# Kernel tuning notes

Hardware: AMD Instinct MI355X
Metric: run time of the kernel (lower is better)

## Reference

```python
import jax, jax.numpy as jnp
import numpy as np

# Sizes (see shape_source): B=4, N1=8192, N2=4096, T=H1=15, E1=131072, E2=65536
# conv1: Fin=1, G1=64, K=12, H=15 (collapse_H=True -> temporal dim folds to 1)
# conv2: Fin=64, G2=32, K=12, H=1

def _cheb_norm(src, dst, w, n):
    # Scaled Laplacian with lambda_max=2 (PyG ChebConv sym norm): L_hat = -D^{-1/2} A D^{-1/2}
    deg = jax.ops.segment_sum(w, dst, num_segments=n)
    dinv = jnp.where(deg > 0, 1.0 / jnp.sqrt(deg), 0.0)
    return -w * dinv[src] * dinv[dst]

def _prop(h, src, dst, norm, n):
    # h: (N, D, B) -> (L_hat h): (N, D, B) via edge gather + segment-sum scatter
    return jax.ops.segment_sum(norm[:, None, None] * h[src], dst, num_segments=n)

def _cheb_time_conv(h, src, dst, norm, W, b, n):
    # Chebyshev recursion: T0=x, T1=L_hat x, Tk = 2 L_hat T_{k-1} - T_{k-2}
    # h: (N, D, B); W: (K, D, G); output (N, G, B). D folds temporal H and Fin.
    K = W.shape[0]
    y = jnp.einsum('ndb,dg->ngb', h, W[0])
    Tx_prev = h
    Tx_cur = _prop(h, src, dst, norm, n)
    y = y + jnp.einsum('ndb,dg->ngb', Tx_cur, W[1])
    for k in range(2, K):
        Tx_next = 2.0 * _prop(Tx_cur, src, dst, norm, n) - Tx_prev
        y = y + jnp.einsum('ndb,dg->ngb', Tx_next, W[k])
        Tx_prev, Tx_cur = Tx_cur, Tx_next
    return y + b[None, :, None]

def setup_inputs() -> dict:
    key = jax.random.key(0)
    ks = jax.random.split(key, 12)
    B, N1, N2, T = 4, 8192, 4096, 15
    E1, E2 = 131072, 65536
    K, G1, G2, C = 12, 64, 32, 6
    return {
        'x': jax.random.normal(ks[0], (B, N1, T), dtype=jnp.float32),
        'edge_index1': jax.random.randint(ks[1], (2, E1), 0, N1, dtype=jnp.int64),
        'edge_weight1': jax.random.uniform(ks[2], (E1,), dtype=jnp.float32),
        'edge_index2': jax.random.randint(ks[3], (2, E2), 0, N2, dtype=jnp.int64),
        'edge_weight2': jax.random.uniform(ks[4], (E2,), dtype=jnp.float32),
        'b_map': jax.random.normal(ks[5], (N2, N1), dtype=jnp.float32) * 0.02,
        'W1': jax.random.normal(ks[6], (K, T, 1, G1), dtype=jnp.float32) * 0.1,
        'b1': jax.random.normal(ks[7], (G1,), dtype=jnp.float32) * 0.1,
        'W2': jax.random.normal(ks[8], (K, 1, G1, G2), dtype=jnp.float32) * 0.05,
        'b2': jax.random.normal(ks[9], (G2,), dtype=jnp.float32) * 0.1,
        'fc_w': jax.random.normal(ks[10], (C, N2 * G2), dtype=jnp.float32) * 0.01,
        'fc_b': jax.random.normal(ks[11], (C,), dtype=jnp.float32) * 0.1,
    }

def reference(x, edge_index1, edge_weight1, edge_index2, edge_weight2,
              b_map, W1, b1, W2, b2, fc_w, fc_b):
    Bsz = x.shape[0]
    h = jnp.transpose(x, (1, 2, 0))                      # torch x.permute(1,2,0): (N1, T, B)
    n1 = h.shape[0]
    s1, d1 = edge_index1[0], edge_index1[1]
    norm1 = _cheb_norm(s1, d1, edge_weight1, n1)
    # conv1: collapse_H folds the whole T=H window -> (N1, G1, B)
    h = _cheb_time_conv(h, s1, d1, norm1, W1.reshape(W1.shape[0], -1, W1.shape[-1]), b1, n1)
    h = jax.nn.relu(h)
    # temporal/pooling mapping: torch.matmul(b, x.permute(2,3,0,1)).permute(2,3,0,1)
    h = jnp.einsum('mn,ngb->mgb', b_map, h)              # (N2, G1, B)
    n2 = h.shape[0]
    s2, d2 = edge_index2[0], edge_index2[1]
    norm2 = _cheb_norm(s2, d2, edge_weight2, n2)
    h = _cheb_time_conv(h, s2, d2, norm2, W2.reshape(W2.shape[0], -1, W2.shape[-1]), b2, n2)  # (N2, G2, B)
    # faithful torch .view(B, -1) on contiguous (N2, G2, 1, B)
    flat = jnp.reshape(h[:, :, None, :], (Bsz, -1))
    logits = flat @ fc_w.T + fc_b
    return jax.nn.log_softmax(logits, axis=1)
```

## Files before the change

### kernel.cpp

```cpp
#include <hip/hip_runtime.h>

#define NB   4
#define NN1  8192
#define TT   15
#define NN2  4096
#define KCH  12
#define GG1  64
#define GG2  32
#define NCLS 6
#define EE1  131072
#define EE2  65536

typedef __attribute__((ext_vector_type(8))) short bf16x8;
typedef __attribute__((ext_vector_type(4))) float f32x4;

__device__ inline short f2bf(float f) {
    unsigned u = __builtin_bit_cast(unsigned, f);
    u += 0x7FFFu + ((u >> 16) & 1u);
    return (short)(u >> 16);
}

__global__ void k_deg_hist(const int* __restrict__ ei, const float* __restrict__ w,
                           float* __restrict__ deg, int* __restrict__ cnt, int E) {
    int e = blockIdx.x * 256 + threadIdx.x;
    if (e < E) {
        int d = ei[E + e];
        atomicAdd(&deg[d], w[e]);
        atomicAdd(&cnt[d], 1);
    }
}

template <int N>
__global__ __launch_bounds__(1024) void k_scan(const int* __restrict__ cnt,
                                               int* __restrict__ offs, int* __restrict__ cur) {
    constexpr int PER = N / 1024;
    __shared__ int part[1024];
    int t = threadIdx.x;
    int loc[PER];
    int s = 0;
#pragma unroll
    for (int i = 0; i < PER; ++i) { loc[i] = s; s += cnt[t * PER + i]; }
    part[t] = s;
    __syncthreads();
    for (int off = 1; off < 1024; off <<= 1) {
        int v = (t >= off) ? part[t - off] : 0;
        __syncthreads();
        part[t] += v;
        __syncthreads();
    }
    int pre = t ? part[t - 1] : 0;
#pragma unroll
    for (int i = 0; i < PER; ++i) { int v = pre + loc[i]; offs[t * PER + i] = v; cur[t * PER + i] = v; }
    if (t == 1023) offs[N] = part[1023];
}

__global__ void k_fill(const int* __restrict__ ei, const float* __restrict__ w,
                       const float* __restrict__ deg, int* __restrict__ cur,
                       int* __restrict__ csrc, float* __restrict__ cnrm, int E) {
    int e = blockIdx.x * 256 + threadIdx.x;
    if (e < E) {
        int s = ei[e], d = ei[E + e];
        float ds = deg[s], dd = deg[d];
        float is = ds > 0.f ? 1.f / sqrtf(ds) : 0.f;
        float id = dd > 0.f ? 1.f / sqrtf(dd) : 0.f;
        int p = atomicAdd(&cur[d], 1);
        csrc[p] = s;
        cnrm[p] = -w[e] * is * id;
    }
}

__global__ void k_build_h0(const float* __restrict__ x, float* __restrict__ h0,
                           short* __restrict__ bf0) {
    int idx = blockIdx.x * 256 + threadIdx.x;
    if (idx < NN1 * 64) {
        int n = idx >> 6, r = idx & 63;
        float v = 0.f;
        if (r < 60) {
            int t = r >> 2, b = r & 3;
            v = x[(b * NN1 + n) * TT + t];
        }
        h0[idx] = v;
        bf0[(size_t)n * 768 + r] = f2bf(v);
    }
}

__global__ __launch_bounds__(64) void k_prop1(const float* __restrict__ hprev,
                                              const float* __restrict__ hprev2,
                                              float* __restrict__ hout, short* __restrict__ bfs,
                                              const int* __restrict__ offs,
                                              const int* __restrict__ csrc,
                                              const float* __restrict__ cnrm, int first) {
    int n = blockIdx.x;
    int lane = threadIdx.x;
    int es = lane >> 4, f4 = lane & 15;
    int e0 = offs[n], e1 = offs[n + 1];
    f32x4 acc = {0.f, 0.f, 0.f, 0.f};
    for (int e = e0 + es; e < e1; e += 4) {
        int s = csrc[e];
        float wv = cnrm[e];
        const float4 v = *(const float4*)(hprev + (size_t)s * 64 + f4 * 4);
        acc[0] = fmaf(wv, v.x, acc[0]);
        acc[1] = fmaf(wv, v.y, acc[1]);
        acc[2] = fmaf(wv, v.z, acc[2]);
        acc[3] = fmaf(wv, v.w, acc[3]);
    }
#pragma unroll
    for (int i = 0; i < 4; ++i) {
        acc[i] += __shfl_xor(acc[i], 16, 64);
        acc[i] += __shfl_xor(acc[i], 32, 64);
    }
    if (es == 0) {
        float4 t;
        if (first) {
            t = make_float4(acc[0], acc[1], acc[2], acc[3]);
        } else {
            float4 p = *(const float4*)(hprev2 + (size_t)n * 64 + f4 * 4);
            t = make_float4(2.f * acc[0] - p.x, 2.f * acc[1] - p.y,
                            2.f * acc[2] - p.z, 2.f * acc[3] - p.w);
        }
        *(float4*)(hout + (size_t)n * 64 + f4 * 4) = t;
        short4 s4;
        s4.x = f2bf(t.x); s4.y = f2bf(t.y); s4.z = f2bf(t.z); s4.w = f2bf(t.w);
        *(short4*)(bfs + (size_t)n * 768 + f4 * 4) = s4;
    }
}

__global__ __launch_bounds__(256) void k_prop2(const float* __restrict__ hprev,
                                               const float* __restrict__ hprev2,
                                               float* __restrict__ hout, short* __restrict__ bfs,
                                               const int* __restrict__ offs,
                                               const int* __restrict__ csrc,
                                               const float* __restrict__ cnrm, int first) {
    __shared__ f32x4 red[3][64];
    int n = blockIdx.x;
    int t = threadIdx.x;
    int w = t >> 6, lane = t & 63;
    int e0 = offs[n], e1 = offs[n + 1];
    f32x4 acc = {0.f, 0.f, 0.f, 0.f};
    for (int e = e0 + w; e < e1; e += 4) {
        int s = csrc[e];
        float wv = cnrm[e];
        const float4 v = *(const float4*)(hprev + (size_t)s * 256 + lane * 4);
        acc[0] = fmaf(wv, v.x, acc[0]);
        acc[1] = fmaf(wv, v.y, acc[1]);
        acc[2] = fmaf(wv, v.z, acc[2]);
        acc[3] = fmaf(wv, v.w, acc[3]);
    }
    if (w) red[w - 1][lane] = acc;
    __syncthreads();
    if (w == 0) {
        f32x4 s = acc + red[0][lane] + red[1][lane] + red[2][lane];
        float4 tt;
        if (first) {
            tt = make_float4(s[0], s[1], s[2], s[3]);
        } else {
            float4 p = *(const float4*)(hprev2 + (size_t)n * 256 + lane * 4);
            tt = make_float4(2.f * s[0] - p.x, 2.f * s[1] - p.y,
                             2.f * s[2] - p.z, 2.f * s[3] - p.w);
        }
        *(float4*)(hout + (size_t)n * 256 + lane * 4) = tt;
        short4 s4;
        s4.x = f2bf(tt.x); s4.y = f2bf(tt.y); s4.z = f2bf(tt.z); s4.w = f2bf(tt.w);
        *(short4*)(bfs + (size_t)n * 3072 + lane * 4) = s4;
    }
}

__global__ void k_w1p(const float* __restrict__ W1, short* __restrict__ W1p) {
    int idx = blockIdx.x * 256 + threadIdx.x;
    if (idx < 256 * 768) {
        int j = idx / 768, d = idx - j * 768;
        int g = j >> 2, b = j & 3;
        int k = d >> 6, r = d & 63, t = r >> 2, bp = r & 3;
        float v = (b == bp && t < TT) ? W1[k * (TT * GG1) + t * GG1 + g] : 0.f;
        W1p[idx] = f2bf(v);
    }
}
__global__ void k_w2p(const float* __restrict__ W2, short* __restrict__ W2p) {
    int idx = blockIdx.x * 256 + threadIdx.x;
    if (idx < 128 * 3072) {
        int j = idx / 3072, d = idx - j * 3072;
        int g = j >> 2, b = j & 3;
        int k = d >> 8, r = d & 255, G = r >> 2, bp = r & 3;
        float v = (b == bp) ? W2[k * (GG1 * GG2) + G * GG2 + g] : 0.f;
        W2p[idx] = f2bf(v);
    }
}

template <bool A_BF, bool Y1EPI>
__global__ __launch_bounds__(256) void k_gemm(const void* __restrict__ Ap, int lda,
                                              const short* __restrict__ Bp, int ldb,
                                              const float* __restrict__ bias,
                                              float* __restrict__ Cf, int ldc,
                                              short* __restrict__ yT,
                                              int Kc, size_t pstride) {
    __shared__ short As[2][64][64];
    __shared__ short Bs[2][64][64];
    int m0 = blockIdx.x * 64, j0 = blockIdx.y * 64;
    int z = blockIdx.z;
    int kbeg = z * Kc;
    float* C = Cf + (size_t)z * pstride;
    int t = threadIdx.x;
    int lane = t & 63, wid = t >> 6;
    int wm = (wid >> 1) * 32, wn = (wid & 1) * 32;
    int lc = lane & 15, kg = lane >> 4;
    int r4 = t >> 2, c4 = (t & 3) * 16;
    int swa = (r4 & 7) << 3;

    const float* apf = (const float*)Ap + (size_t)(m0 + r4) * lda + kbeg + (t & 3) * 4;
    const short* apb = (const short*)Ap + (size_t)(m0 + r4) * lda + kbeg + c4;
    const short* bp  = Bp + (size_t)(j0 + r4) * ldb + kbeg + c4;

    float4 af0, af1, af2, af3;
    bf16x8 ab0, ab1, bb0, bb1;

    auto load_tile = [&](int k0) {
        if (A_BF) {
            ab0 = *(const bf16x8*)(apb + k0);
            ab1 = *(const bf16x8*)(apb + k0 + 8);
        } else {
            af0 = *(const float4*)(apf + k0);
            af1 = *(const float4*)(apf + k0 + 16);
            af2 = *(const float4*)(apf + k0 + 32);
            af3 = *(const float4*)(apf + k0 + 48);
        }
        bb0 = *(const bf16x8*)(bp + k0);
        bb1 = *(const bf16x8*)(bp + k0 + 8);
    };
    auto write_tile = [&](int buf) {
        if (A_BF) {
            *(bf16x8*)&As[buf][r4][c4 ^ swa] = ab0;
            *(bf16x8*)&As[buf][r4][(c4 + 8) ^ swa] = ab1;
        } else {
            short4 s;
            s.x = f2bf(af0.x); s.y = f2bf(af0.y); s.z = f2bf(af0.z); s.w = f2bf(af0.w);
            *(short4*)&As[buf][r4][((t & 3) * 4) ^ swa] = s;
            s.x = f2bf(af1.x); s.y = f2bf(af1.y); s.z = f2bf(af1.z); s.w = f2bf(af1.w);
            *(short4*)&As[buf][r4][((t & 3) * 4 + 16) ^ swa] = s;
            s.x = f2bf(af2.x); s.y = f2bf(af2.y); s.z = f2bf(af2.z); s.w = f2bf(af2.w);
            *(short4*)&As[buf][r4][((t & 3) * 4 + 32) ^ swa] = s;
            s.x = f2bf(af3.x); s.y = f2bf(af3.y); s.z = f2bf(af3.z); s.w = f2bf(af3.w);
            *(short4*)&As[buf][r4][((t & 3) * 4 + 48) ^ swa] = s;
        }
        *(bf16x8*)&Bs[buf][r4][c4 ^ swa] = bb0;
        *(bf16x8*)&Bs[buf][r4][(c4 + 8) ^ swa] = bb1;
    };

    f32x4 acc[2][2] = {};
    const int NIT = Kc >> 6;
    load_tile(0);
    write_tile(0);
    __syncthreads();
    for (int it = 0; it < NIT; ++it) {
        int cur = it & 1;
        if (it + 1 < NIT) load_tile((it + 1) << 6);
#pragma unroll
        for (int ks = 0; ks < 2; ++ks) {
            int kk = ks * 32 + kg * 8;
            bf16x8 a[2], b[2];
#pragma unroll
            for (int mi = 0; mi < 2; ++mi) {
                int row = wm + mi * 16 + lc;
                a[mi] = *(bf16x8*)&As[cur][row][kk ^ ((row & 7) << 3)];
            }
#pragma unroll
            for (int ni = 0; ni < 2; ++ni) {
                int row = wn + ni * 16 + lc;
                b[ni] = *(bf16x8*)&Bs[cur][row][kk ^ ((row & 7) << 3)];
            }
#pragma unroll
            for (int mi = 0; mi < 2; ++mi)
#pragma unroll
                for (int ni = 0; ni < 2; ++ni)
                    acc[mi][ni] = __builtin_amdgcn_mfma_f32_16x16x32_bf16(a[mi], b[ni], acc[mi][ni], 0, 0, 0);
        }
        if (it + 1 < NIT) write_tile(cur ^ 1);
        __syncthreads();
    }

    if (Y1EPI) {
#pragma unroll
        for (int mi = 0; mi < 2; ++mi)
#pragma unroll
            for (int ni = 0; ni < 2; ++ni) {
                int col = j0 + wn + ni * 16 + lc;
                float bb = bias[col >> 2];
                int row = m0 + wm + mi * 16 + kg * 4;
                short4 s;
                s.x = f2bf(fmaxf(acc[mi][ni][0] + bb, 0.f));
                s.y = f2bf(fmaxf(acc[mi][ni][1] + bb, 0.f));
                s.z = f2bf(fmaxf(acc[mi][ni][2] + bb, 0.f));
                s.w = f2bf(fmaxf(acc[mi][ni][3] + bb, 0.f));
                *(short4*)(yT + (size_t)col * NN1 + row) = s;
            }
    } else {
#pragma unroll
        for (int mi = 0; mi < 2; ++mi)
#pragma unroll
            for (int ni = 0; ni < 2; ++ni)
#pragma unroll
                for (int r = 0; r < 4; ++r) {
                    int row = m0 + wm + mi * 16 + kg * 4 + r, col = j0 + wn + ni * 16 + lc;
                    C[(size_t)row * ldc + col] = acc[mi][ni][r];
                }
    }
}

__global__ void k_red8(const float* __restrict__ part, float* __restrict__ Cf,
                       short* __restrict__ Cbf) {
    int i = blockIdx.x * 256 + threadIdx.x;
    if (i < NN2 * 64) {
        const float4* p = (const float4*)part + i;
        float4 s = p[0];
#pragma unroll
        for (int z = 1; z < 8; ++z) {
            float4 v = p[(size_t)z * NN2 * 64];
            s.x += v.x; s.y += v.y; s.z += v.z; s.w += v.w;
        }
        ((float4*)Cf)[i] = s;
        int n = i >> 6, col = (i & 63) * 4;
        short4 s4;
        s4.x = f2bf(s.x); s4.y = f2bf(s.y); s4.z = f2bf(s.z); s4.w = f2bf(s.w);
        *(short4*)(Cbf + (size_t)n * 3072 + col) = s4;
    }
}
__global__ void k_red4(const float* __restrict__ part, float* __restrict__ Cf) {
    int i = blockIdx.x * 256 + threadIdx.x;
    if (i < NN2 * 32) {
        const float4* p = (const float4*)part + i;
        float4 s = p[0];
#pragma unroll
        for (int z = 1; z < 4; ++z) {
            float4 v = p[(size_t)z * NN2 * 32];
            s.x += v.x; s.y += v.y; s.z += v.z; s.w += v.w;
        }
        ((float4*)Cf)[i] = s;
    }
}

__global__ __launch_bounds__(256) void k_fc(const float* __restrict__ y2, const float* __restrict__ b2,
                                            const float* __restrict__ fcw, float* __restrict__ logits) {
    int qc = blockIdx.x >> 4, ch = blockIdx.x & 15;
    int q = qc / NCLS, c = qc % NCLS;
    const float* yp = y2 + (size_t)q * 131072 + ch * 8192;
    const float* wp = fcw + (size_t)c * 131072 + ch * 8192;
    int t = threadIdx.x;
    float acc = 0.f;
#pragma unroll
    for (int it = 0; it < 8; ++it) {
        int o = it * 1024 + t * 4;
        float4 yv = *(const float4*)(yp + o);
        float4 wv = *(const float4*)(wp + o);
        float bg = b2[((ch * 8192 + o) >> 2) & 31];
        acc += (yv.x + bg) * wv.x + (yv.y + bg) * wv.y + (yv.z + bg) * wv.z + (yv.w + bg) * wv.w;
    }
#pragma unroll
    for (int o = 32; o; o >>= 1) acc += __shfl_down(acc, o, 64);
    __shared__ float red[4];
    if ((t & 63) == 0) red[t >> 6] = acc;
    __syncthreads();
    if (t == 0) atomicAdd(&logits[qc], red[0] + red[1] + red[2] + red[3]);
}

__global__ void k_lsm(const float* __restrict__ logits, const float* __restrict__ fcb,
                      float* __restrict__ out) {
    int q = threadIdx.x;
    if (q < NB) {
        float v[NCLS];
#pragma unroll
        for (int c = 0; c < NCLS; ++c) v[c] = logits[q * NCLS + c] + fcb[c];
        float m = -1e30f;
#pragma unroll
        for (int c = 0; c < NCLS; ++c) m = fmaxf(m, v[c]);
        float s = 0.f;
#pragma unroll
        for (int c = 0; c < NCLS; ++c) s += expf(v[c] - m);
        float lse = m + logf(s);
#pragma unroll
        for (int c = 0; c < NCLS; ++c) out[q * NCLS + c] = v[c] - lse;
    }
}

extern "C" void kernel_launch(void* const* d_in, const int* in_sizes, int n_in,
                              void* d_out, int out_size, void* d_ws, size_t ws_size,
                              hipStream_t stream) {
    const float* x    = (const float*)d_in[0];
    const int*   ei1  = (const int*)d_in[1];
    const float* ew1  = (const float*)d_in[2];
    const int*   ei2  = (const int*)d_in[3];
    const float* ew2  = (const float*)d_in[4];
    const float* bmap = (const float*)d_in[5];
    const float* W1   = (const float*)d_in[6];
    const float* b1   = (const float*)d_in[7];
    const float* W2   = (const float*)d_in[8];
    const float* b2   = (const float*)d_in[9];
    const float* fcw  = (const float*)d_in[10];
    const float* fcb  = (const float*)d_in[11];
    float* out = (float*)d_out;

    char* w = (char*)d_ws;
    size_t o = 0;
    auto alloc = [&](size_t bytes) {
        char* p = w + o;
        o += (bytes + 255) & ~(size_t)255;
        return p;
    };
    float* deg1  = (float*)alloc(NN1 * 4);
    float* deg2  = (float*)alloc(NN2 * 4);
    int*   cnt1  = (int*)alloc(NN1 * 4);
    int*   cnt2  = (int*)alloc(NN2 * 4);
    int*   offs1 = (int*)alloc((NN1 + 1) * 4);
    int*   offs2 = (int*)alloc((NN2 + 1) * 4);
    int*   cur1  = (int*)alloc(NN1 * 4);
    int*   cur2  = (int*)alloc(NN2 * 4);
    int*   csrc1 = (int*)alloc(EE1 * 4);
    float* cnrm1 = (float*)alloc(EE1 * 4);
    int*   csrc2 = (int*)alloc(EE2 * 4);
    float* cnrm2 = (float*)alloc(EE2 * 4);
    float* R1a = (float*)alloc(NN1 * 64 * 4);
    float* R1b = (float*)alloc(NN1 * 64 * 4);
    float* R1c = (float*)alloc(NN1 * 64 * 4);
    short* T1bf = (short*)alloc((size_t)NN1 * 768 * 2);
    short* ybfT = (short*)alloc((size_t)256 * NN1 * 2);
    float* R2a = (float*)alloc((size_t)NN2 * 256 * 4);
    float* R2b = (float*)alloc((size_t)NN2 * 256 * 4);
    float* R2c = (float*)alloc((size_t)NN2 * 256 * 4);
    short* T2bf = (short*)alloc((size_t)NN2 * 3072 * 2);
    float* y2  = (float*)alloc((size_t)NN2 * 128 * 4);
    short* W1p = (short*)alloc(256 * 768 * 2);
    short* W2p = (short*)alloc(128 * 3072 * 2);
    float* part8 = (float*)alloc((size_t)8 * NN2 * 256 * 4);
    float* part4 = (float*)alloc((size_t)4 * NN2 * 128 * 4);
    float* logits = (float*)alloc(256);

    hipMemsetAsync(deg1, 0, NN1 * 4, stream);
    hipMemsetAsync(deg2, 0, NN2 * 4, stream);
    hipMemsetAsync(cnt1, 0, NN1 * 4, stream);
    hipMemsetAsync(cnt2, 0, NN2 * 4, stream);
    hipMemsetAsync(logits, 0, 256, stream);
    k_deg_hist<<<EE1 / 256, 256, 0, stream>>>(ei1, ew1, deg1, cnt1, EE1);
    k_deg_hist<<<EE2 / 256, 256, 0, stream>>>(ei2, ew2, deg2, cnt2, EE2);
    k_scan<NN1><<<1, 1024, 0, stream>>>(cnt1, offs1, cur1);
    k_scan<NN2><<<1, 1024, 0, stream>>>(cnt2, offs2, cur2);
    k_fill<<<EE1 / 256, 256, 0, stream>>>(ei1, ew1, deg1, cur1, csrc1, cnrm1, EE1);
    k_fill<<<EE2 / 256, 256, 0, stream>>>(ei2, ew2, deg2, cur2, csrc2, cnrm2, EE2);

    k_w1p<<<(256 * 768) / 256, 256, 0, stream>>>(W1, W1p);
    k_w2p<<<(128 * 3072) / 256, 256, 0, stream>>>(W2, W2p);

    k_build_h0<<<(NN1 * 64) / 256, 256, 0, stream>>>(x, R1a, T1bf);
    {
        float *Tm1 = R1a, *Tm2 = nullptr, *fr = R1b, *spare = R1c;
        for (int k = 1; k < KCH; ++k) {
            k_prop1<<<NN1, 64, 0, stream>>>(Tm1, k == 1 ? Tm1 : Tm2, fr,
                                            T1bf + k * 64, offs1, csrc1, cnrm1, k == 1 ? 1 : 0);
            float* nf = (k == 1) ? spare : Tm2;
            Tm2 = Tm1; Tm1 = fr; fr = nf;
        }
    }
    {
        dim3 g(NN1 / 64, 256 / 64, 1);
        k_gemm<true, true><<<g, 256, 0, stream>>>(T1bf, 768, W1p, 768, b1,
                                                  nullptr, 0, ybfT, 768, 0);
    }
    {
        dim3 g(NN2 / 64, 256 / 64, 8);
        k_gemm<false, false><<<g, 256, 0, stream>>>(bmap, NN1, ybfT, NN1, nullptr,
                                                    part8, 256, nullptr, 1024, (size_t)NN2 * 256);
        k_red8<<<(NN2 * 64 + 255) / 256, 256, 0, stream>>>(part8, R2a, T2bf);
    }
    {
        float *Tm1 = R2a, *Tm2 = nullptr, *fr = R2b, *spare = R2c;
        for (int k = 1; k < KCH; ++k) {
            k_prop2<<<NN2, 256, 0, stream>>>(Tm1, k == 1 ? Tm1 : Tm2, fr,
                                             T2bf + k * 256, offs2, csrc2, cnrm2, k == 1 ? 1 : 0);
            float* nf = (k == 1) ? spare : Tm2;
            Tm2 = Tm1; Tm1 = fr; fr = nf;
        }
    }
    {
        dim3 g(NN2 / 64, 128 / 64, 4);
        k_gemm<true, false><<<g, 256, 0, stream>>>(T2bf, 3072, W2p, 3072, nullptr,
                                                   part4, 128, nullptr, 768, (size_t)NN2 * 128);
        k_red4<<<(NN2 * 32 + 255) / 256, 256, 0, stream>>>(part4, y2);
    }

    k_fc<<<NB * NCLS * 16, 256, 0, stream>>>(y2, b2, fcw, logits);
    k_lsm<<<1, 64, 0, stream>>>(logits, fcb, out);
}
```

Before: 555.3 us.

## Add 128x128 double-buffered MFMA GEMM for b_map mapping, pack node propagation kernels

Replaces the generic 64x64 GEMM for the dense b_map x conv1 output product with a dedicated 128x128 tile kernel. It converts fp32 A to bf16 on the fly, double-buffers LDS with an XOR swizzle, and prefetches the next K tile into registers during the MFMA work, which raises data reuse and hides load latency. The propagation kernels now pack four nodes per 256-thread block. k_prop2 handles one node per wave with a 2-way unrolled edge loop instead of splitting edges across waves and reducing through LDS. The tradeoff is higher register pressure in the big-tile GEMM and less edge-level parallelism per node in prop2.

New measurement: 559.3 us. No clear change (+0.7%).

```diff
diff --git a/kernel.cpp b/kernel.cpp
--- a/kernel.cpp
+++ b/kernel.cpp
@@ -18,6 +18,12 @@
     unsigned u = __builtin_bit_cast(unsigned, f);
     u += 0x7FFFu + ((u >> 16) & 1u);
     return (short)(u >> 16);
+}
+__device__ inline bf16x8 cvt8(float4 a, float4 b) {
+    bf16x8 r;
+    r[0] = f2bf(a.x); r[1] = f2bf(a.y); r[2] = f2bf(a.z); r[3] = f2bf(a.w);
+    r[4] = f2bf(b.x); r[5] = f2bf(b.y); r[6] = f2bf(b.z); r[7] = f2bf(b.w);
+    return r;
 }
 
 __global__ void k_deg_hist(const int* __restrict__ ei, const float* __restrict__ w,
@@ -84,14 +90,14 @@
     }
 }
 
-__global__ __launch_bounds__(64) void k_prop1(const float* __restrict__ hprev,
-                                              const float* __restrict__ hprev2,
-                                              float* __restrict__ hout, short* __restrict__ bfs,
-                                              const int* __restrict__ offs,
-                                              const int* __restrict__ csrc,
-                                              const float* __restrict__ cnrm, int first) {
-    int n = blockIdx.x;
-    int lane = threadIdx.x;
+__global__ __launch_bounds__(256) void k_prop1(const float* __restrict__ hprev,
+                                               const float* __restrict__ hprev2,
+                                               float* __restrict__ hout, short* __restrict__ bfs,
+                                               const int* __restrict__ offs,
+                                               const int* __restrict__ csrc,
+                                               const float* __restrict__ cnrm, int first) {
+    int n = blockIdx.x * 4 + (threadIdx.x >> 6);
+    int lane = threadIdx.x & 63;
     int es = lane >> 4, f4 = lane & 15;
     int e0 = offs[n], e1 = offs[n + 1];
     f32x4 acc = {0.f, 0.f, 0.f, 0.f};
@@ -131,38 +137,41 @@
                                                const int* __restrict__ offs,
                                                const int* __restrict__ csrc,
                                                const float* __restrict__ cnrm, int first) {
-    __shared__ f32x4 red[3][64];
-    int n = blockIdx.x;
-    int t = threadIdx.x;
-    int w = t >> 6, lane = t & 63;
+    int n = blockIdx.x * 4 + (threadIdx.x >> 6);
+    int lane = threadIdx.x & 63;
     int e0 = offs[n], e1 = offs[n + 1];
-    f32x4 acc = {0.f, 0.f, 0.f, 0.f};
-    for (int e = e0 + w; e < e1; e += 4) {
-        int s = csrc[e];
-        float wv = cnrm[e];
-        const float4 v = *(const float4*)(hprev + (size_t)s * 256 + lane * 4);
-        acc[0] = fmaf(wv, v.x, acc[0]);
-        acc[1] = fmaf(wv, v.y, acc[1]);
-        acc[2] = fmaf(wv, v.z, acc[2]);
-        acc[3] = fmaf(wv, v.w, acc[3]);
-    }
-    if (w) red[w - 1][lane] = acc;
-    __syncthreads();
-    if (w == 0) {
-        f32x4 s = acc + red[0][lane] + red[1][lane] + red[2][lane];
-        float4 tt;
-        if (first) {
-            tt = make_float4(s[0], s[1], s[2], s[3]);
-        } else {
-            float4 p = *(const float4*)(hprev2 + (size_t)n * 256 + lane * 4);
-            tt = make_float4(2.f * s[0] - p.x, 2.f * s[1] - p.y,
-                             2.f * s[2] - p.z, 2.f * s[3] - p.w);
-        }
-        *(float4*)(hout + (size_t)n * 256 + lane * 4) = tt;
-        short4 s4;
-        s4.x = f2bf(tt.x); s4.y = f2bf(tt.y); s4.z = f2bf(tt.z); s4.w = f2bf(tt.w);
-        *(short4*)(bfs + (size_t)n * 3072 + lane * 4) = s4;
-    }
+    f32x4 a0 = {0.f, 0.f, 0.f, 0.f}, a1 = {0.f, 0.f, 0.f, 0.f};
+    int e = e0;
+    for (; e + 1 < e1; e += 2) {
+        int s0 = csrc[e], s1 = csrc[e + 1];
+        float w0 = cnrm[e], w1 = cnrm[e + 1];
+        float4 v0 = *(const float4*)(hprev + (size_t)s0 * 256 + lane * 4);
+        float4 v1 = *(const float4*)(hprev + (size_t)s1 * 256 + lane * 4);
+        a0[0] = fmaf(w0, v0.x, a0[0]); a0[1] = fmaf(w0, v0.y, a0[1]);
+        a0[2] = fmaf(w0, v0.z, a0[2]); a0[3] = fmaf(w0, v0.w, a0[3]);
+        a1[0] = fmaf(w1, v1.x, a1[0]); a1[1] = fmaf(w1, v1.y, a1[1]);
+        a1[2] = fmaf(w1, v1.z, a1[2]); a1[3] = fmaf(w1, v1.w, a1[3]);
+    }
+    if (e < e1) {
+        int s0 = csrc[e];
+        float w0 = cnrm[e];
+        float4 v0 = *(const float4*)(hprev + (size_t)s0 * 256 + lane * 4);
+        a0[0] = fmaf(w0, v0.x, a0[0]); a0[1] = fmaf(w0, v0.y, a0[1]);
+        a0[2] = fmaf(w0, v0.z, a0[2]); a0[3] = fmaf(w0, v0.w, a0[3]);
+    }
+    f32x4 s = a0 + a1;
+    float4 tt;
+    if (first) {
+        tt = make_float4(s[0], s[1], s[2], s[3]);
+    } else {
+        float4 p = *(const float4*)(hprev2 + (size_t)n * 256 + lane * 4);
+        tt = make_float4(2.f * s[0] - p.x, 2.f * s[1] - p.y,
+                         2.f * s[2] - p.z, 2.f * s[3] - p.w);
+    }
+    *(float4*)(hout + (size_t)n * 256 + lane * 4) = tt;
+    short4 s4;
+    s4.x = f2bf(tt.x); s4.y = f2bf(tt.y); s4.z = f2bf(tt.z); s4.w = f2bf(tt.w);
+    *(short4*)(bfs + (size_t)n * 3072 + lane * 4) = s4;
 }
 
 __global__ void k_w1p(const float* __restrict__ W1, short* __restrict__ W1p) {
@@ -303,6 +312,87 @@
                     C[(size_t)row * ldc + col] = acc[mi][ni][r];
                 }
     }
+}
+
+__global__ __launch_bounds__(256) void k_gemm128(const float* __restrict__ Ap,
+                                                 const short* __restrict__ Bp,
+                                                 float* __restrict__ Cf,
+                                                 int Kc, size_t pstride) {
+    __shared__ short As[2][128][64];
+    __shared__ short Bs[2][128][64];
+    int m0 = blockIdx.x * 128, j0 = blockIdx.y * 128;
+    int z = blockIdx.z;
+    int kbeg = z * Kc;
+    float* C = Cf + (size_t)z * pstride;
+    int t = threadIdx.x;
+    int lane = t & 63, wid = t >> 6;
+    int wr = (wid >> 1) * 64, wc = (wid & 1) * 64;
+    int lc = lane & 15, kg = lane >> 4;
+    int rs = t >> 1;
+    int hb = (t & 1) * 32;
+    int swa = (rs & 7) << 3;
+
+    const float* ap = Ap + (size_t)(m0 + rs) * NN1 + kbeg + hb;
+    const short* bp = Bp + (size_t)(j0 + rs) * NN1 + kbeg + hb;
+
+    float4 af[8];
+    bf16x8 bb[4];
+    auto load_tile = [&](int k0) {
+#pragma unroll
+        for (int q = 0; q < 8; ++q) af[q] = *(const float4*)(ap + k0 + q * 4);
+#pragma unroll
+        for (int q = 0; q < 4; ++q) bb[q] = *(const bf16x8*)(bp + k0 + q * 8);
+    };
+    auto write_tile = [&](int buf) {
+#pragma unroll
+        for (int q = 0; q < 4; ++q)
+            *(bf16x8*)&As[buf][rs][(hb + q * 8) ^ swa] = cvt8(af[2 * q], af[2 * q + 1]);
+#pragma unroll
+        for (int q = 0; q < 4; ++q)
+            *(bf16x8*)&Bs[buf][rs][(hb + q * 8) ^ swa] = bb[q];
+    };
+
+    f32x4 acc[4][4] = {};
+    const int NIT = Kc >> 6;
+    load_tile(0);
+    write_tile(0);
+    __syncthreads();
+    for (int it = 0; it < NIT; ++it) {
+        int cur = it & 1;
+        if (it + 1 < NIT) load_tile((it + 1) << 6);
+#pragma unroll
+        for (int ks = 0; ks < 2; ++ks) {
+            int kk = ks * 32 + kg * 8;
+            bf16x8 a[4], b[4];
+#pragma unroll
+            for (int mi = 0; mi < 4; ++mi) {
+                int row = wr + mi * 16 + lc;
+                a[mi] = *(bf16x8*)&As[cur][row][kk ^ ((row & 7) << 3)];
+            }
+#pragma unroll
+            for (int ni = 0; ni < 4; ++ni) {
+                int row = wc + ni * 16 + lc;
+                b[ni] = *(bf16x8*)&Bs[cur][row][kk ^ ((row & 7) << 3)];
+            }
+#pragma unroll
+            for (int mi = 0; mi < 4; ++mi)
+#pragma unroll
+                for (int ni = 0; ni < 4; ++ni)
+                    acc[mi][ni] = __builtin_amdgcn_mfma_f32_16x16x32_bf16(a[mi], b[ni], acc[mi][ni], 0, 0, 0);
+        }
+        if (it + 1 < NIT) write_tile(cur ^ 1);
+        __syncthreads();
+    }
+#pragma unroll
+    for (int mi = 0; mi < 4; ++mi)
+#pragma unroll
+        for (int ni = 0; ni < 4; ++ni)
+#pragma unroll
+            for (int r = 0; r < 4; ++r) {
+                int row = m0 + wr + mi * 16 + kg * 4 + r;
+                int col = j0 + wc + ni * 16 + lc;
+                C[(size_t)row * 256 + col] = acc[mi][ni][r];
+            }
 }
 
 __global__ void k_red8(const float* __restrict__ part, float* __restrict__ Cf,
@@ -451,8 +541,8 @@
     {
         float *Tm1 = R1a, *Tm2 = nullptr, *fr = R1b, *spare = R1c;
         for (int k = 1; k < KCH; ++k) {
-            k_prop1<<<NN1, 64, 0, stream>>>(Tm1, k == 1 ? Tm1 : Tm2, fr,
-                                            T1bf + k * 64, offs1, csrc1, cnrm1, k == 1 ? 1 : 0);
+            k_prop1<<<NN1 / 4, 256, 0, stream>>>(Tm1, k == 1 ? Tm1 : Tm2, fr,
+                                                 T1bf + k * 64, offs1, csrc1, cnrm1, k == 1 ? 1 : 0);
             float* nf = (k == 1) ? spare : Tm2;
             Tm2 = Tm1; Tm1 = fr; fr = nf;
         }
@@ -463,16 +553,15 @@
                                                   nullptr, 0, ybfT, 768, 0);
     }
     {
-        dim3 g(NN2 / 64, 256 / 64, 8);
-        k_gemm<false, false><<<g, 256, 0, stream>>>(bmap, NN1, ybfT, NN1, nullptr,
-                                                    part8, 256, nullptr, 1024, (size_t)NN2 * 256);
+        dim3 g(NN2 / 128, 256 / 128, 8);
+        k_gemm128<<<g, 256, 0, stream>>>(bmap, ybfT, part8, 1024, (size_t)NN2 * 256);
         k_red8<<<(NN2 * 64 + 255) / 256, 256, 0, stream>>>(part8, R2a, T2bf);
     }
     {
         float *Tm1 = R2a, *Tm2 = nullptr, *fr = R2b, *spare = R2c;
         for (int k = 1; k < KCH; ++k) {
-            k_prop2<<<NN2, 256, 0, stream>>>(Tm1, k == 1 ? Tm1 : Tm2, fr,
-                                             T2bf + k * 256, offs2, csrc2, cnrm2, k == 1 ? 1 : 0);
+            k_prop2<<<NN2 / 4, 256, 0, stream>>>(Tm1, k == 1 ? Tm1 : Tm2, fr,
+                                                 T2bf + k * 256, offs2, csrc2, cnrm2, k == 1 ? 1 : 0);
             float* nf = (k == 1) ? spare : Tm2;
             Tm2 = Tm1; Tm1 = fr; fr = nf;
         }
```
